# Kernel optimization log

Measured on AMD Instinct MI355X. Metric: run time of the kernel, lower is better.

Reference implementation:

```python
import math
import jax, jax.numpy as jnp
import numpy as np

B, T, E, H = 4, 4096, 512, 8
D = E // H
TOP_K = int(3 * math.log(T))  # autocorrelation_factor * log(time_length) = 24


def setup_inputs() -> dict:
    key = jax.random.key(0)
    ks = jax.random.split(key, 9)
    s = 0.02
    return {
        "hidden_states": jax.random.normal(ks[0], (B, T, E), jnp.float32),
        "Wq": jax.random.normal(ks[1], (E, E), jnp.float32) * s,
        "bq": jax.random.normal(ks[2], (E,), jnp.float32) * s,
        "Wk": jax.random.normal(ks[3], (E, E), jnp.float32) * s,
        "bk": jax.random.normal(ks[4], (E,), jnp.float32) * s,
        "Wv": jax.random.normal(ks[5], (E, E), jnp.float32) * s,
        "bv": jax.random.normal(ks[6], (E,), jnp.float32) * s,
        "Wo": jax.random.normal(ks[7], (E, E), jnp.float32) * s,
        "bo": jax.random.normal(ks[8], (E,), jnp.float32) * s,
    }


def _heads(x):
    # [B,T,E] -> [B*H,T,D] (b-major over heads, matching torch view/transpose/reshape)
    return x.reshape(B, T, H, D).transpose(0, 2, 1, 3).reshape(B * H, T, D)


def reference(hidden_states, Wq, bq, Wk, bk, Wv, bv, Wo, bo):
    q = _heads(hidden_states @ Wq.T + bq)
    k = _heads(hidden_states @ Wk.T + bk)
    v = _heads(hidden_states @ Wv.T + bv)

    # FFT-based autocorrelation: irfft(rfft(q) * conj(rfft(k)))  -> [B*H,T,D]
    qf = jnp.fft.rfft(q, n=T, axis=1)
    kf = jnp.fft.rfft(k, n=T, axis=1)
    ac = jnp.fft.irfft(qf * jnp.conj(kf), n=T, axis=1)

    # mean over heads and channels -> [B,T]; eval-mode per-batch top-k delays
    ac_mean = ac.reshape(B, H, T, D).mean(axis=(1, 3))
    top_vals, top_idx = jax.lax.top_k(ac_mean, TOP_K)      # [B,K]
    w = jax.nn.softmax(top_vals, axis=-1)                  # [B,K]

    # torch .repeat(num_heads,...) tiles batch entries: row j uses batch j % B
    w_t = jnp.tile(w, (H, 1))        # [B*H,K]
    d_t = jnp.tile(top_idx, (H, 1))  # [B*H,K]

    t = jnp.arange(T)
    agg = jnp.zeros_like(v)
    for i in range(TOP_K):
        idx = (t[None, :] + d_t[:, i:i + 1]) % T           # circular shift by -delay
        rolled = jnp.take_along_axis(v, idx[:, :, None], axis=1)
        agg = agg + w_t[:, i][:, None, None] * rolled

    out = agg.reshape(B, H, T, D).transpose(0, 2, 1, 3).reshape(B, T, E)
    return out @ Wo.T + bo
```

## Files before the change

### kernel.cpp

```cpp
#include <hip/hip_runtime.h>
#include <math.h>

#define B_ 4
#define T_ 4096
#define E_ 512
#define H_ 8
#define TOPK 24
#define FH 2049
#define FHP 2064
#define F2 2064
#define ZROWS 16512
#define NRH 16384

typedef __attribute__((ext_vector_type(8))) short bf16x8;
typedef __attribute__((ext_vector_type(4))) float f32x4;

__device__ __forceinline__ unsigned short f2bf(float f) {
    unsigned u = __float_as_uint(f);
    u = (u + 0x7FFFu + ((u >> 16) & 1u)) >> 16;
    return (unsigned short)u;
}
__device__ __forceinline__ float bf2f(unsigned short h) {
    return __uint_as_float(((unsigned)h) << 16);
}
__device__ __forceinline__ void glds16(const unsigned short* g, short* l) {
    __builtin_amdgcn_global_load_lds(
        (const __attribute__((address_space(1))) unsigned int*)g,
        (__attribute__((address_space(3))) unsigned int*)l, 16, 0, 0);
}


__global__ __launch_bounds__(256) void trsp_split(const float* __restrict__ hid,
                                                  float* __restrict__ Htr,
                                                  unsigned short* __restrict__ Ah)
{
    __shared__ float tile[64][68];
    const int b = blockIdx.z;
    const int t0 = blockIdx.x * 64, e0 = blockIdx.y * 64;
    const int r = threadIdx.x >> 4;
    const int c4 = (threadIdx.x & 15) * 4;
#pragma unroll
    for (int s = 0; s < 4; s++) {
        int t = t0 + r + 16 * s;
        float4 v = *(const float4*)&hid[((size_t)b * T_ + t) * E_ + e0 + c4];
        tile[r + 16 * s][c4 + 0] = v.x; tile[r + 16 * s][c4 + 1] = v.y;
        tile[r + 16 * s][c4 + 2] = v.z; tile[r + 16 * s][c4 + 3] = v.w;
        ushort4 hv = make_ushort4(f2bf(v.x), f2bf(v.y), f2bf(v.z), f2bf(v.w));
        int e = e0 + c4;
        int rowg = b * T_ + t;
        *(ushort4*)&Ah[((size_t)(e >> 3) * NRH + rowg) * 8 + (e & 7)] = hv;
    }
    __syncthreads();
#pragma unroll
    for (int s = 0; s < 4; s++) {
        int e = e0 + r + 16 * s;
        float4 o;
        o.x = tile[c4 + 0][r + 16 * s];
        o.y = tile[c4 + 1][r + 16 * s];
        o.z = tile[c4 + 2][r + 16 * s];
        o.w = tile[c4 + 3][r + 16 * s];
        *(float4*)&Htr[((size_t)b * E_ + e) * T_ + t0 + c4] = o;
    }
}

__global__ __launch_bounds__(256) void split_w2(const float* __restrict__ wv,
                                                const float* __restrict__ wo,
                                                unsigned short* __restrict__ Wvh,
                                                unsigned short* __restrict__ Woh)
{
    const float* src = blockIdx.y ? wo : wv;
    unsigned short* dst = blockIdx.y ? Woh : Wvh;
    int i = (blockIdx.x * 256 + threadIdx.x) * 4;
    int m = i >> 9, k = i & 511;
    float4 v = *(const float4*)&src[i];
    *(ushort4*)&dst[((size_t)(k >> 3) * 512 + m) * 8 + (k & 7)] =
        make_ushort4(f2bf(v.x), f2bf(v.y), f2bf(v.z), f2bf(v.w));
}

__global__ __launch_bounds__(256) void wprep_partial(const float* __restrict__ Wq,
                                                     const float* __restrict__ Wk,
                                                     float* __restrict__ Mp)
{
    __shared__ float As[8][132];
    __shared__ float Bs[8][132];
    const int j0 = blockIdx.x * 128, k0 = blockIdx.y * 128;
    const int e0 = blockIdx.z * 32;
    const int tid = threadIdx.x;
    const int tm = tid & 15, tn = tid >> 4;
    const int le = tid >> 5, lc = (tid & 31) * 4;
    float acc[8][8];
#pragma unroll
    for (int i = 0; i < 8; i++)
#pragma unroll
        for (int j = 0; j < 8; j++) acc[i][j] = 0.f;
    for (int eb = e0; eb < e0 + 32; eb += 8) {
        __syncthreads();
        *(float4*)&As[le][lc] = *(const float4*)&Wq[((size_t)(eb + le)) * 512 + k0 + lc];
        *(float4*)&Bs[le][lc] = *(const float4*)&Wk[((size_t)(eb + le)) * 512 + j0 + lc];
        __syncthreads();
#pragma unroll
        for (int e = 0; e < 8; e++) {
            float a[8], bb[8];
            *(float4*)&a[0] = *(float4*)&As[e][4 * tn];
            *(float4*)&a[4] = *(float4*)&As[e][64 + 4 * tn];
            *(float4*)&bb[0] = *(float4*)&Bs[e][4 * tm];
            *(float4*)&bb[4] = *(float4*)&Bs[e][64 + 4 * tm];
#pragma unroll
            for (int i = 0; i < 8; i++)
#pragma unroll
                for (int j = 0; j < 8; j++)
                    acc[i][j] += a[i] * bb[j];
        }
    }
    float* out = Mp + (size_t)blockIdx.z * 512 * 512;
#pragma unroll
    for (int jj = 0; jj < 8; jj++) {
        int j = j0 + ((jj < 4) ? (4 * tm + jj) : (64 + 4 * tm + jj - 4));
        float4 o0 = make_float4(acc[0][jj], acc[1][jj], acc[2][jj], acc[3][jj]);
        float4 o1 = make_float4(acc[4][jj], acc[5][jj], acc[6][jj], acc[7][jj]);
        *(float4*)&out[(size_t)j * 512 + k0 + 4 * tn] = o0;
        *(float4*)&out[(size_t)j * 512 + k0 + 64 + 4 * tn] = o1;
    }
}

__global__ __launch_bounds__(256) void reduce_split_m(const float* __restrict__ Mp,
                                                      unsigned short* __restrict__ Mth,
                                                      unsigned short* __restrict__ Mtl)
{
    int i = (blockIdx.x * 256 + threadIdx.x) * 4;
    if (i >= 512 * 512) return;
    float4 s = make_float4(0.f, 0.f, 0.f, 0.f);
#pragma unroll
    for (int z = 0; z < 16; z++) {
        float4 v = *(const float4*)&Mp[(size_t)z * 262144 + i];
        s.x += v.x; s.y += v.y; s.z += v.z; s.w += v.w;
    }
    int j = i >> 9, k = i & 511;
    float f[4] = {s.x, s.y, s.z, s.w};
    unsigned short hh[4], ll[4];
#pragma unroll
    for (int r = 0; r < 4; r++) {
        hh[r] = f2bf(f[r]);
        ll[r] = f2bf(f[r] - bf2f(hh[r]));
    }
    size_t o = ((size_t)(k >> 3) * 512 + j) * 8 + (k & 7);
    *(ushort4*)&Mth[o] = make_ushort4(hh[0], hh[1], hh[2], hh[3]);
    *(ushort4*)&Mtl[o] = make_ushort4(ll[0], ll[1], ll[2], ll[3]);
}

template<int PASSES, int OMODE, int HASBIAS>
__device__ __forceinline__ void gemm_body(const unsigned short* __restrict__ Ah,
                                          const unsigned short* __restrict__ Al, int nrA,
                                          const unsigned short* __restrict__ Bh,
                                          const unsigned short* __restrict__ Bl,
                                          const float* __restrict__ bias,
                                          void* __restrict__ Cp,
                                          int m0, int n0, short* smem)
{
    const int tid = threadIdx.x;
    const int wid = tid >> 6, lane = tid & 63;
    const int wn = wid >> 1, wm = wid & 1;
    const int lr = lane & 15, lg = lane >> 4;
    constexpr int SEGW = (PASSES == 3) ? 8 : 4;
    constexpr int BUFSZ = (PASSES == 3) ? 16384 : 8192;

    f32x4 acc[4][4];
#pragma unroll
    for (int i = 0; i < 4; i++)
#pragma unroll
        for (int j = 0; j < 4; j++) acc[i][j] = (f32x4)0.f;

    auto stage = [&](int kc0, short* buf) {
#pragma unroll
        for (int s = 0; s < SEGW; s++) {
            const int sg = wid * SEGW + s;
            const int tile = sg >> 3;
            const int seg = sg & 7;
            const int c = seg >> 1, h = seg & 1;
            const unsigned short* bp;
            size_t ro;
            if (tile == 0)      { bp = Ah; ro = (size_t)(kc0 + c) * (size_t)nrA + n0 + h * 64; }
            else if (tile == 1) { bp = Bh; ro = (size_t)(kc0 + c) * 512 + m0 + h * 64; }
            else if (tile == 2) { bp = Al; ro = (size_t)(kc0 + c) * (size_t)nrA + n0 + h * 64; }
            else                { bp = Bl; ro = (size_t)(kc0 + c) * 512 + m0 + h * 64; }
            glds16(bp + ro * 8 + (size_t)lane * 8, buf + tile * 4096 + seg * 512);
        }
    };

    stage(0, smem);
    for (int step = 0; step < 16; step++) {
        short* cur = smem + (step & 1) * BUFSZ;
        short* nxt = smem + ((step + 1) & 1) * BUFSZ;
        __syncthreads();
        if (step < 15) stage((step + 1) * 4, nxt);

        bf16x8 a[4], b[4];
#pragma unroll
        for (int f = 0; f < 4; f++) {
            a[f] = *(bf16x8*)&cur[       (lg * 128 + wn * 64 + f * 16 + lr) * 8];
            b[f] = *(bf16x8*)&cur[4096 + (lg * 128 + wm * 64 + f * 16 + lr) * 8];
        }
        if (PASSES == 3) {
            bf16x8 a2[4], b2[4];
#pragma unroll
            for (int f = 0; f < 4; f++) {
                a2[f] = *(bf16x8*)&cur[8192  + (lg * 128 + wn * 64 + f * 16 + lr) * 8];
                b2[f] = *(bf16x8*)&cur[12288 + (lg * 128 + wm * 64 + f * 16 + lr) * 8];
            }
#pragma unroll
            for (int i = 0; i < 4; i++)
#pragma unroll
                for (int j = 0; j < 4; j++) {
                    acc[i][j] = __builtin_amdgcn_mfma_f32_16x16x32_bf16(a[i], b[j], acc[i][j], 0, 0, 0);
                    acc[i][j] = __builtin_amdgcn_mfma_f32_16x16x32_bf16(a[i], b2[j], acc[i][j], 0, 0, 0);
                    acc[i][j] = __builtin_amdgcn_mfma_f32_16x16x32_bf16(a2[i], b[j], acc[i][j], 0, 0, 0);
                }
        } else {
#pragma unroll
            for (int i = 0; i < 4; i++)
#pragma unroll
                for (int j = 0; j < 4; j++)
                    acc[i][j] = __builtin_amdgcn_mfma_f32_16x16x32_bf16(a[i], b[j], acc[i][j], 0, 0, 0);
        }
    }

    float bs[4];
#pragma unroll
    for (int j = 0; j < 4; j++) bs[j] = HASBIAS ? bias[m0 + wm * 64 + j * 16 + lr] : 0.f;

    if (OMODE == 0) {
        float* C = (float*)Cp;
#pragma unroll
        for (int i = 0; i < 4; i++)
#pragma unroll
            for (int j = 0; j < 4; j++) {
                int m = m0 + wm * 64 + j * 16 + lr;
#pragma unroll
                for (int r = 0; r < 4; r++) {
                    int n = n0 + wn * 64 + i * 16 + lg * 4 + r;
                    C[(size_t)n * 512 + m] = acc[i][j][r] + bs[j];
                }
            }
    } else {
        unsigned short* C = (unsigned short*)Cp;
#pragma unroll
        for (int i = 0; i < 4; i++)
#pragma unroll
            for (int j = 0; j < 4; j++) {
                int m = m0 + wm * 64 + j * 16 + lr;
#pragma unroll
                for (int r = 0; r < 4; r++) {
                    int n = n0 + wn * 64 + i * 16 + lg * 4 + r;
                    C[(size_t)n * 512 + m] = f2bf(acc[i][j][r] + bs[j]);
                }
            }
    }
}

__global__ __launch_bounds__(256) void fused_vy(const unsigned short* __restrict__ Ah,
                                                const unsigned short* __restrict__ Wvh,
                                                const float* __restrict__ bv,
                                                unsigned short* __restrict__ Vb,
                                                const unsigned short* __restrict__ Zh,
                                                const unsigned short* __restrict__ Zl,
                                                const unsigned short* __restrict__ Mth,
                                                const unsigned short* __restrict__ Mtl,
                                                float* __restrict__ Y)
{
    __shared__ short smem[32768];
    const int m0 = blockIdx.x * 128;
    const int n0 = blockIdx.y * 128;
    if (blockIdx.z == 0) {
        if (blockIdx.y >= 128) return;
        gemm_body<1, 2, 1>(Ah, Ah, NRH, Wvh, Wvh, bv, Vb, m0, n0, smem);
    } else {
        gemm_body<3, 0, 0>(Zh, Zl, ZROWS, Mth, Mtl, nullptr, Y, m0, n0, smem);
    }
}

__global__ __launch_bounds__(256) void o_gemm(const unsigned short* __restrict__ Ag,
                                              const unsigned short* __restrict__ Woh,
                                              const float* __restrict__ bo,
                                              float* __restrict__ C)
{
    __shared__ short smem[16384];
    gemm_body<1, 0, 1>(Ag, Ag, NRH, Woh, Woh, bo, C, blockIdx.x * 128, blockIdx.y * 128, smem);
}

template<int SGN>
__device__ __forceinline__ void radix8(float* xr, float* xi)
{
    const float C = 0.70710678118654752440f;
    const float S = (float)SGN;
    float t0r = xr[0] + xr[4], t0i = xi[0] + xi[4];
    float t1r = xr[1] + xr[5], t1i = xi[1] + xi[5];
    float t2r = xr[2] + xr[6], t2i = xi[2] + xi[6];
    float t3r = xr[3] + xr[7], t3i = xi[3] + xi[7];
    float u0r = xr[0] - xr[4], u0i = xi[0] - xi[4];
    float a1r = xr[1] - xr[5], a1i = xi[1] - xi[5];
    float a2r = xr[2] - xr[6], a2i = xi[2] - xi[6];
    float a3r = xr[3] - xr[7], a3i = xi[3] - xi[7];
    float u1r = C * (a1r - S * a1i), u1i = C * (S * a1r + a1i);
    float u2r = -S * a2i,             u2i = S * a2r;
    float u3r = -C * (a3r + S * a3i), u3i = C * (S * a3r - a3i);
    float v0r = t0r + t2r, v0i = t0i + t2i;
    float w0r = t0r - t2r, w0i = t0i - t2i;
    float v1r = t1r + t3r, v1i = t1i + t3i;
    float w1r = -S * (t1i - t3i), w1i = S * (t1r - t3r);
    float p0r = u0r + u2r, p0i = u0i + u2i;
    float q0r = u0r - u2r, q0i = u0i - u2i;
    float p1r = u1r + u3r, p1i = u1i + u3i;
    float q1r = -S * (u1i - u3i), q1i = S * (u1r - u3r);
    xr[0] = v0r + v1r; xi[0] = v0i + v1i;
    xr[4] = v0r - v1r; xi[4] = v0i - v1i;
    xr[2] = w0r + w1r; xi[2] = w0i + w1i;
    xr[6] = w0r - w1r; xi[6] = w0i - w1i;
    xr[1] = p0r + p1r; xi[1] = p0i + p1i;
    xr[5] = p0r - p1r; xi[5] = p0i - p1i;
    xr[3] = q0r + q1r; xi[3] = q0i + q1i;
    xr[7] = q0r - q1r; xi[7] = q0i - q1i;
}

__device__ __forceinline__ void twmul(float& xr, float& xi, float wc, float ws)
{
    float a = xr, b = xi;
    xr = a * wc - b * ws;
    xi = a * ws + b * wc;
}

__device__ __forceinline__ void twiddle7(float* xr, float* xi, int n, float ang)
{
    float s1, c1;
    __sincosf(ang * (float)n, &s1, &c1);
    float wc = c1, ws = s1;
    twmul(xr[1], xi[1], wc, ws);
#pragma unroll
    for (int r = 2; r < 8; r++) {
        float nc = wc * c1 - ws * s1;
        float ns = wc * s1 + ws * c1;
        wc = nc; ws = ns;
        twmul(xr[r], xi[r], wc, ws);
    }
}

#define SW(i) ((i) + ((i) >> 3))

template<int SGN>
__device__ __forceinline__ void fft_core(float* xr, float* xi,
                                         float* lre, float* lim, int tid)
{
    const float TW = (float)SGN * 6.28318530717958647693f;
    __syncthreads();
    radix8<SGN>(xr, xi);
    twiddle7(xr, xi, tid, TW / 4096.f);
#pragma unroll
    for (int r = 0; r < 8; r++) {
        int idx = r * 512 + tid;
        lre[SW(idx)] = xr[r]; lim[SW(idx)] = xi[r];
    }
    __syncthreads();
    const int b2 = (tid >> 6) * 512, n2 = tid & 63;
#pragma unroll
    for (int s = 0; s < 8; s++) {
        int idx = b2 + n2 + s * 64;
        xr[s] = lre[SW(idx)]; xi[s] = lim[SW(idx)];
    }
    __syncthreads();
    radix8<SGN>(xr, xi);
    twiddle7(xr, xi, n2, TW / 512.f);
#pragma unroll
    for (int r = 0; r < 8; r++) {
        int idx = b2 + r * 64 + n2;
        lre[SW(idx)] = xr[r]; lim[SW(idx)] = xi[r];
    }
    __syncthreads();
    const int b3 = (tid >> 3) * 64, n3 = tid & 7;
#pragma unroll
    for (int s = 0; s < 8; s++) {
        int idx = b3 + n3 + s * 8;
        xr[s] = lre[SW(idx)]; xi[s] = lim[SW(idx)];
    }
    __syncthreads();
    radix8<SGN>(xr, xi);
    twiddle7(xr, xi, n3, TW / 64.f);
#pragma unroll
    for (int r = 0; r < 8; r++) {
        int idx = b3 + r * 8 + n3;
        lre[SW(idx)] = xr[r]; lim[SW(idx)] = xi[r];
    }
    __syncthreads();
#pragma unroll
    for (int s = 0; s < 8; s++) {
        int idx = tid * 8 + s;
        xr[s] = lre[SW(idx)]; xi[s] = lim[SW(idx)];
    }
    __syncthreads();
    radix8<SGN>(xr, xi);
    const int fr = ((tid & 7) << 6) | (((tid >> 3) & 7) << 3) | (tid >> 6);
#pragma unroll
    for (int r = 0; r < 8; r++) {
        int f = r * 512 + fr;
        lre[SW(f)] = xr[r]; lim[SW(f)] = xi[r];
    }
    __syncthreads();
}

__global__ __launch_bounds__(512) void fft_fwd_z(const float* __restrict__ Htr,
                                                 unsigned short* __restrict__ Zh,
                                                 unsigned short* __restrict__ Zl)
{
    __shared__ float lre[4608];
    __shared__ float lim[4608];
    const int bid = blockIdx.x;
    const int tid = threadIdx.x;
    const int b = bid >> 7;
    const int e0 = (bid & 127) * 4;
    unsigned uh[4][2][2], ul[4][2][2];
#pragma unroll
    for (int p = 0; p < 2; p++) {
        const float* he = Htr + ((size_t)(b * 512 + e0 + 2 * p)) * 4096;
        const float* ho = Htr + ((size_t)(b * 512 + e0 + 2 * p + 1)) * 4096;
        float xr[8], xi[8];
#pragma unroll
        for (int s = 0; s < 8; s++) {
            xr[s] = he[tid + 512 * s];
            xi[s] = ho[tid + 512 * s];
        }
        fft_core<-1>(xr, xi, lre, lim, tid);
#pragma unroll
        for (int s = 0; s < 4; s++) {
            int f = tid + 512 * s;
            int nf = (4096 - f) & 4095;
            float Ax = lre[SW(f)],  Ay = lim[SW(f)];
            float Bx = lre[SW(nf)], By = lim[SW(nf)];
            float qx = 0.5f * (Ax + Bx), qy = 0.5f * (Ay - By);
            float kx = 0.5f * (Ay + By), ky = -0.5f * (Ax - Bx);
            unsigned short h0 = f2bf(qx), h1 = f2bf(kx);
            uh[s][0][p] = (unsigned)h0 | ((unsigned)h1 << 16);
            ul[s][0][p] = (unsigned)f2bf(qx - bf2f(h0)) | ((unsigned)f2bf(kx - bf2f(h1)) << 16);
            unsigned short h2 = f2bf(qy), h3 = f2bf(ky);
            uh[s][1][p] = (unsigned)h2 | ((unsigned)h3 << 16);
            ul[s][1][p] = (unsigned)f2bf(qy - bf2f(h2)) | ((unsigned)f2bf(ky - bf2f(h3)) << 16);
        }
        if (tid == 0) {
            float vals[2] = {lre[SW(2048)], lim[SW(2048)]};
            size_t row0 = (size_t)(b * 2) * F2 + 2048;
#pragma unroll
            for (int q = 0; q < 2; q++) {
                int e = e0 + 2 * p + q;
                size_t o0 = ((size_t)(e >> 3) * ZROWS + row0) * 8 + (e & 7);
                unsigned short h = f2bf(vals[q]);
                Zh[o0] = h; Zl[o0] = f2bf(vals[q] - bf2f(h));
                size_t o1 = ((size_t)(e >> 3) * ZROWS + row0 + F2) * 8 + (e & 7);
                Zh[o1] = 0; Zl[o1] = 0;
            }
        }
    }
#pragma unroll
    for (int s = 0; s < 4; s++)
#pragma unroll
        for (int c = 0; c < 2; c++) {
            size_t row = (size_t)(b * 2 + c) * F2 + tid + 512 * s;
            size_t off = ((size_t)(e0 >> 3) * ZROWS + row) * 8 + (e0 & 7);
            ushort4 vh = make_ushort4((unsigned short)(uh[s][c][0] & 0xffff),
                                      (unsigned short)(uh[s][c][0] >> 16),
                                      (unsigned short)(uh[s][c][1] & 0xffff),
                                      (unsigned short)(uh[s][c][1] >> 16));
            ushort4 vl = make_ushort4((unsigned short)(ul[s][c][0] & 0xffff),
                                      (unsigned short)(ul[s][c][0] >> 16),
                                      (unsigned short)(ul[s][c][1] & 0xffff),
                                      (unsigned short)(ul[s][c][1] >> 16));
            *(ushort4*)&Zh[off] = vh;
            *(ushort4*)&Zl[off] = vl;
        }
}

__global__ __launch_bounds__(256) void dot_s(const float* __restrict__ Y,
                                             const unsigned short* __restrict__ Zh,
                                             const unsigned short* __restrict__ Zl,
                                             float2* __restrict__ Sp)
{
    const int f = blockIdx.x * 256 + threadIdx.x;
    const int b = blockIdx.y;
    const int gz = blockIdx.z;
    if (f > 2048) return;
    const size_t row_re = (size_t)(b * 2) * F2 + f;
    const size_t row_im = row_re + F2;
    float sre = 0.f, sim = 0.f;
    for (int c = gz * 4; c < gz * 4 + 4; c++) {
        bf16x8 zrh = *(const bf16x8*)&Zh[((size_t)c * ZROWS + row_re) * 8];
        bf16x8 zrl = *(const bf16x8*)&Zl[((size_t)c * ZROWS + row_re) * 8];
        bf16x8 zih = *(const bf16x8*)&Zh[((size_t)c * ZROWS + row_im) * 8];
        bf16x8 zil = *(const bf16x8*)&Zl[((size_t)c * ZROWS + row_im) * 8];
        float4 yr0 = *(const float4*)&Y[row_re * 512 + c * 8];
        float4 yr1 = *(const float4*)&Y[row_re * 512 + c * 8 + 4];
        float4 yi0 = *(const float4*)&Y[row_im * 512 + c * 8];
        float4 yi1 = *(const float4*)&Y[row_im * 512 + c * 8 + 4];
        float yrv[8] = {yr0.x, yr0.y, yr0.z, yr0.w, yr1.x, yr1.y, yr1.z, yr1.w};
        float yiv[8] = {yi0.x, yi0.y, yi0.z, yi0.w, yi1.x, yi1.y, yi1.z, yi1.w};
#pragma unroll
        for (int j = 0; j < 8; j++) {
            float zr = bf2f((unsigned short)zrh[j]) + bf2f((unsigned short)zrl[j]);
            float zi = bf2f((unsigned short)zih[j]) + bf2f((unsigned short)zil[j]);
            sre += yrv[j] * zr + yiv[j] * zi;
            sim += yiv[j] * zr - yrv[j] * zi;
        }
    }
    Sp[((size_t)gz * 4 + b) * FHP + f] = make_float2(sre, sim);
}

__global__ __launch_bounds__(512) void ifft_kernel(const float2* __restrict__ Sp,
                                                   float* __restrict__ acm)
{
    __shared__ float lre[4608];
    __shared__ float lim[4608];
    const int b = blockIdx.x, tid = threadIdx.x;
    float xr[8], xi[8];
#pragma unroll
    for (int s = 0; s < 8; s++) {
        int idx = tid + 512 * s;
        int src = (idx <= 2048) ? idx : (4096 - idx);
        float sx = 0.f, sy = 0.f;
#pragma unroll
        for (int gz = 0; gz < 16; gz++) {
            float2 v = Sp[((size_t)gz * 4 + b) * FHP + src];
            sx += v.x; sy += v.y;
        }
        xr[s] = sx;
        xi[s] = (idx <= 2048) ? sy : -sy;
    }
    fft_core<1>(xr, xi, lre, lim, tid);
    const float scale = 1.0f / ((float)T_ * (float)E_);
#pragma unroll
    for (int s = 0; s < 8; s++) {
        int p = tid + 512 * s;
        acm[b * T_ + p] = lre[SW(p)] * scale;
    }
}

__global__ __launch_bounds__(256) void topk_kernel(const float* __restrict__ acm,
                                                   int* __restrict__ delays,
                                                   float* __restrict__ weights)
{
    __shared__ float vals[4096];
    __shared__ float bv[256];
    __shared__ int   bi[256];
    __shared__ float topv[TOPK];
    const int b = blockIdx.x, tid = threadIdx.x;
#pragma unroll
    for (int s = 0; s < 16; s++) vals[tid + 256 * s] = acm[b * T_ + tid + 256 * s];
    __syncthreads();
    for (int it = 0; it < TOPK; it++) {
        float best = -INFINITY; int bidx = 0;
#pragma unroll
        for (int s = 0; s < 16; s++) {
            int idx = tid * 16 + s;
            float v = vals[idx];
            if (v > best) { best = v; bidx = idx; }
        }
        bv[tid] = best; bi[tid] = bidx;
        __syncthreads();
        for (int off = 128; off > 0; off >>= 1) {
            if (tid < off) {
                if (bv[tid + off] > bv[tid] ||
                    (bv[tid + off] == bv[tid] && bi[tid + off] < bi[tid])) {
                    bv[tid] = bv[tid + off]; bi[tid] = bi[tid + off];
                }
            }
            __syncthreads();
        }
        if (tid == 0) {
            delays[b * TOPK + it] = bi[0];
            topv[it] = bv[0];
            vals[bi[0]] = -INFINITY;
        }
        __syncthreads();
    }
    if (tid == 0) {
        float mx = topv[0];
        float w[TOPK], sum = 0.f;
        for (int i = 0; i < TOPK; i++) { w[i] = expf(topv[i] - mx); sum += w[i]; }
        for (int i = 0; i < TOPK; i++) weights[b * TOPK + i] = w[i] / sum;
    }
}

__global__ __launch_bounds__(256) void agg_kernel(const unsigned short* __restrict__ V,
                                                  const int* __restrict__ delays,
                                                  const float* __restrict__ wts,
                                                  unsigned short* __restrict__ agg)
{
    __shared__ int   dly[B_][TOPK];
    __shared__ float wt[B_][TOPK];
    const int tid = threadIdx.x, b = blockIdx.y;
    if (tid < B_ * TOPK) {
        dly[tid / TOPK][tid % TOPK] = delays[tid];
        wt[tid / TOPK][tid % TOPK]  = wts[tid];
    }
    __syncthreads();
    const int lane = tid & 63, w = tid >> 6;
    const int t = blockIdx.x * 4 + w;
    const int e8 = lane * 8;
    const int h = e8 >> 6;
    const int c = (b * H_ + h) % B_;
    const unsigned short* Vb = V + (size_t)b * T_ * E_;
    float acc[8];
#pragma unroll
    for (int j = 0; j < 8; j++) acc[j] = 0.f;
#pragma unroll
    for (int i = 0; i < TOPK; i++) {
        int tt = (t + dly[c][i]) & (T_ - 1);
        bf16x8 v = *(const bf16x8*)&Vb[(size_t)tt * E_ + e8];
        float wg = wt[c][i];
#pragma unroll
        for (int j = 0; j < 8; j++)
            acc[j] += wg * bf2f((unsigned short)v[j]);
    }
    bf16x8 o;
#pragma unroll
    for (int j = 0; j < 8; j++) o[j] = (short)f2bf(acc[j]);
    int rowg = b * T_ + t;
    *(bf16x8*)&agg[((size_t)(e8 >> 3) * NRH + rowg) * 8] = o;
}

extern "C" void kernel_launch(void* const* d_in, const int* in_sizes, int n_in,
                              void* d_out, int out_size, void* d_ws, size_t ws_size,
                              hipStream_t stream)
{
    const float* hidden = (const float*)d_in[0];
    const float* Wq = (const float*)d_in[1];
    const float* Wk = (const float*)d_in[3];
    const float* Wv = (const float*)d_in[5]; const float* bv = (const float*)d_in[6];
    const float* Wo = (const float*)d_in[7]; const float* bo = (const float*)d_in[8];

    char* ws = (char*)d_ws;
    const size_t YA_OFF  = 0;
    const size_t AH_OFF  = 33816576;
    const size_t ZH_OFF  = 50593792;
    const size_t ZL_OFF  = 67502080;
    const size_t VB_OFF  = 84410368;
    const size_t MTH_OFF = 101187584;
    const size_t MTL_OFF = 101711872;
    const size_t WVH_OFF = 102236160;
    const size_t WOH_OFF = 102760448;
    const size_t SP_OFF  = 103284736;
    const size_t ACM_OFF = 104341504;
    const size_t DEL_OFF = 104407040;
    const size_t WTS_OFF = 104407424;
    if (ws_size < 104407808) return;

    float* Htr = (float*)(ws + YA_OFF);
    float* Y   = (float*)(ws + YA_OFF);
    unsigned short* Ah  = (unsigned short*)(ws + AH_OFF);
    unsigned short* Ag  = (unsigned short*)(ws + AH_OFF);
    unsigned short* Zh  = (unsigned short*)(ws + ZH_OFF);
    unsigned short* Zl  = (unsigned short*)(ws + ZL_OFF);
    float* Mp           = (float*)(ws + VB_OFF);
    unsigned short* Vb  = (unsigned short*)(ws + VB_OFF);
    unsigned short* Mth = (unsigned short*)(ws + MTH_OFF);
    unsigned short* Mtl = (unsigned short*)(ws + MTL_OFF);
    unsigned short* Wvh = (unsigned short*)(ws + WVH_OFF);
    unsigned short* Woh = (unsigned short*)(ws + WOH_OFF);
    float2* Sp   = (float2*)(ws + SP_OFF);
    float*  acm  = (float*)(ws + ACM_OFF);
    int*    delays = (int*)(ws + DEL_OFF);
    float*  wts    = (float*)(ws + WTS_OFF);

    dim3 tg(64, 8, 4);
    trsp_split<<<tg, 256, 0, stream>>>(hidden, Htr, Ah);
    dim3 swg(256, 2);
    split_w2<<<swg, 256, 0, stream>>>(Wv, Wo, Wvh, Woh);
    dim3 mg(4, 4, 16);
    wprep_partial<<<mg, 256, 0, stream>>>(Wq, Wk, Mp);
    reduce_split_m<<<256, 256, 0, stream>>>(Mp, Mth, Mtl);

    fft_fwd_z<<<512, 512, 0, stream>>>(Htr, Zh, Zl);

    dim3 gf(4, 129, 2);
    fused_vy<<<gf, 256, 0, stream>>>(Ah, Wvh, bv, Vb, Zh, Zl, Mth, Mtl, Y);

    dim3 dg(9, 4, 16);
    dot_s<<<dg, 256, 0, stream>>>(Y, Zh, Zl, Sp);

    ifft_kernel<<<B_, 512, 0, stream>>>(Sp, acm);
    topk_kernel<<<B_, 256, 0, stream>>>(acm, delays, wts);
    dim3 ag(T_ / 4, B_);
    agg_kernel<<<ag, 256, 0, stream>>>(Vb, delays, wts, Ag);
    dim3 go(4, 128);
    o_gemm<<<go, 256, 0, stream>>>(Ag, Woh, bo, (float*)d_out);
}
```

Baseline: 243.2 us.

## Fuse inverse FFT with top-k selection using register-held values and wave shuffles

```diff
diff --git a/kernel.cpp b/kernel.cpp
--- a/kernel.cpp
+++ b/kernel.cpp
@@ -210,11 +210,18 @@
 #pragma unroll
             for (int i = 0; i < 4; i++)
 #pragma unroll
-                for (int j = 0; j < 4; j++) {
+                for (int j = 0; j < 4; j++)
                     acc[i][j] = __builtin_amdgcn_mfma_f32_16x16x32_bf16(a[i], b[j], acc[i][j], 0, 0, 0);
+#pragma unroll
+            for (int i = 0; i < 4; i++)
+#pragma unroll
+                for (int j = 0; j < 4; j++)
                     acc[i][j] = __builtin_amdgcn_mfma_f32_16x16x32_bf16(a[i], b2[j], acc[i][j], 0, 0, 0);
+#pragma unroll
+            for (int i = 0; i < 4; i++)
+#pragma unroll
+                for (int j = 0; j < 4; j++)
                     acc[i][j] = __builtin_amdgcn_mfma_f32_16x16x32_bf16(a2[i], b[j], acc[i][j], 0, 0, 0);
-                }
         } else {
 #pragma unroll
             for (int i = 0; i < 4; i++)
@@ -509,11 +516,16 @@
     Sp[((size_t)gz * 4 + b) * FHP + f] = make_float2(sre, sim);
 }
 
-__global__ __launch_bounds__(512) void ifft_kernel(const float2* __restrict__ Sp,
-                                                   float* __restrict__ acm)
+__global__ __launch_bounds__(512) void ifft_topk(const float2* __restrict__ Sp,
+                                                 int* __restrict__ delays,
+                                                 float* __restrict__ weights)
 {
     __shared__ float lre[4608];
     __shared__ float lim[4608];
+    __shared__ float bwv[8];
+    __shared__ int   bwi[8];
+    __shared__ float topv[TOPK];
+    __shared__ int   wini;
     const int b = blockIdx.x, tid = threadIdx.x;
     float xr[8], xi[8];
 #pragma unroll
@@ -530,51 +542,40 @@
         xi[s] = (idx <= 2048) ? sy : -sy;
     }
     fft_core<1>(xr, xi, lre, lim, tid);
+
     const float scale = 1.0f / ((float)T_ * (float)E_);
-#pragma unroll
-    for (int s = 0; s < 8; s++) {
-        int p = tid + 512 * s;
-        acm[b * T_ + p] = lre[SW(p)] * scale;
-    }
-}
-
-__global__ __launch_bounds__(256) void topk_kernel(const float* __restrict__ acm,
-                                                   int* __restrict__ delays,
-                                                   float* __restrict__ weights)
-{
-    __shared__ float vals[4096];
-    __shared__ float bv[256];
-    __shared__ int   bi[256];
-    __shared__ float topv[TOPK];
-    const int b = blockIdx.x, tid = threadIdx.x;
-#pragma unroll
-    for (int s = 0; s < 16; s++) vals[tid + 256 * s] = acm[b * T_ + tid + 256 * s];
-    __syncthreads();
+    const int base = tid * 8;
+    float v[8];
+#pragma unroll
+    for (int s = 0; s < 8; s++) v[s] = lre[SW(base + s)] * scale;
+
+    const int wid = tid >> 6, lane = tid & 63;
     for (int it = 0; it < TOPK; it++) {
         float best = -INFINITY; int bidx = 0;
 #pragma unroll
-        for (int s = 0; s < 16; s++) {
-            int idx = tid * 16 + s;
-            float v = vals[idx];
-            if (v > best) { best = v; bidx = idx; }
-        }
-        bv[tid] = best; bi[tid] = bidx;
+        for (int s = 0; s < 8; s++) {
+            if (v[s] > best) { best = v[s]; bidx = base + s; }
+        }
+#pragma unroll
+        for (int off = 32; off > 0; off >>= 1) {
+            float ov = __shfl_down(best, off);
+            int   oi = __shfl_down(bidx, off);
+            if (ov > best || (ov == best && oi < bidx)) { best = ov; bidx = oi; }
+        }
+        if (lane == 0) { bwv[wid] = best; bwi[wid] = bidx; }
         __syncthreads();
-        for (int off = 128; off > 0; off >>= 1) {
-            if (tid < off) {
-                if (bv[tid + off] > bv[tid] ||
-                    (bv[tid + off] == bv[tid] && bi[tid + off] < bi[tid])) {
-                    bv[tid] = bv[tid + off]; bi[tid] = bi[tid + off];
-                }
-            }
-            __syncthreads();
-        }
         if (tid == 0) {
-            delays[b * TOPK + it] = bi[0];
-            topv[it] = bv[0];
-            vals[bi[0]] = -INFINITY;
+            float bv2 = bwv[0]; int bi2 = bwi[0];
+#pragma unroll
+            for (int w = 1; w < 8; w++)
+                if (bwv[w] > bv2 || (bwv[w] == bv2 && bwi[w] < bi2)) { bv2 = bwv[w]; bi2 = bwi[w]; }
+            topv[it] = bv2;
+            delays[b * TOPK + it] = bi2;
+            wini = bi2;
         }
         __syncthreads();
+        int wi = wini;
+        if ((wi >> 3) == tid) v[wi & 7] = -INFINITY;
     }
     if (tid == 0) {
         float mx = topv[0];
@@ -643,10 +644,9 @@
     const size_t WVH_OFF = 102236160;
     const size_t WOH_OFF = 102760448;
     const size_t SP_OFF  = 103284736;
-    const size_t ACM_OFF = 104341504;
-    const size_t DEL_OFF = 104407040;
-    const size_t WTS_OFF = 104407424;
-    if (ws_size < 104407808) return;
+    const size_t DEL_OFF = 104341504;
+    const size_t WTS_OFF = 104341888;
+    if (ws_size < 104342272) return;
 
     float* Htr = (float*)(ws + YA_OFF);
     float* Y   = (float*)(ws + YA_OFF);
@@ -661,7 +661,6 @@
     unsigned short* Wvh = (unsigned short*)(ws + WVH_OFF);
     unsigned short* Woh = (unsigned short*)(ws + WOH_OFF);
     float2* Sp   = (float2*)(ws + SP_OFF);
-    float*  acm  = (float*)(ws + ACM_OFF);
     int*    delays = (int*)(ws + DEL_OFF);
     float*  wts    = (float*)(ws + WTS_OFF);
 
@@ -681,8 +680,7 @@
     dim3 dg(9, 4, 16);
     dot_s<<<dg, 256, 0, stream>>>(Y, Zh, Zl, Sp);
 
-    ifft_kernel<<<B_, 512, 0, stream>>>(Sp, acm);
-    topk_kernel<<<B_, 256, 0, stream>>>(acm, delays, wts);
+    ifft_topk<<<B_, 512, 0, stream>>>(Sp, delays, wts);
     dim3 ag(T_ / 4, B_);
     agg_kernel<<<ag, 256, 0, stream>>>(Vb, delays, wts, Ag);
     dim3 go(4, 128);
```

New measurement: 249.1 us. 1.02x slower.
